# Performance work log

Hardware: AMD Instinct MI355X
Metric: run time of the kernel (lower is better)

The kernel has to match this reference:

```python
import jax, jax.numpy as jnp
import numpy as np

DEPTH, DIM, HEADS, DHEAD, MLP, CTX_DIM = 4, 1024, 16, 64, 4096, 1024
INNER = HEADS * DHEAD
SCALE = DHEAD ** -0.5
B, N, M = 4, 1024, 2048


def setup_inputs() -> dict:
    key = jax.random.key(0)
    ks = jax.random.split(key, 16)
    w = lambda k, shape: jax.random.normal(k, shape, dtype=jnp.float32) * 0.02
    return {
        "x": jax.random.normal(ks[0], (B, N, DIM), dtype=jnp.float32),
        "context": jax.random.normal(ks[1], (B, M, CTX_DIM), dtype=jnp.float32),
        "mask": jnp.ones((B, N), dtype=jnp.int32),
        # LayerNorm params: index 0 = pre-self-attn, 1 = pre-cross-attn, 2 = pre-FFN
        "ln_g": jnp.ones((DEPTH, 3, DIM), dtype=jnp.float32),
        "ln_b": jnp.zeros((DEPTH, 3, DIM), dtype=jnp.float32),
        "Wqkv": w(ks[2], (DEPTH, DIM, 3 * INNER)),
        "Wo_sa": w(ks[3], (DEPTH, INNER, DIM)),
        "bo_sa": jnp.zeros((DEPTH, DIM), dtype=jnp.float32),
        "Wkv": w(ks[4], (DEPTH, CTX_DIM, 2 * INNER)),
        "Wq": w(ks[5], (DEPTH, DIM, INNER)),
        "Wo_ca": w(ks[6], (DEPTH, INNER, DIM)),
        "bo_ca": jnp.zeros((DEPTH, DIM), dtype=jnp.float32),
        "W1": w(ks[7], (DEPTH, DIM, MLP)),
        "b1": jnp.zeros((DEPTH, MLP), dtype=jnp.float32),
        "W2": w(ks[8], (DEPTH, MLP, DIM)),
        "b2": jnp.zeros((DEPTH, DIM), dtype=jnp.float32),
    }


def _ln(x, g, b, eps=1e-5):
    mu = jnp.mean(x, axis=-1, keepdims=True)
    var = jnp.var(x, axis=-1, keepdims=True)
    return (x - mu) * jax.lax.rsqrt(var + eps) * g + b


def _split_heads(t):  # [b, n, h*d] -> [b, h, n, d]
    b, n, _ = t.shape
    return t.reshape(b, n, HEADS, DHEAD).transpose(0, 2, 1, 3)


def _merge_heads(t):  # [b, h, n, d] -> [b, n, h*d]
    b, h, n, d = t.shape
    return t.transpose(0, 2, 1, 3).reshape(b, n, h * d)


def _forward(x, context, mask, ln_g, ln_b, Wqkv, Wo_sa, bo_sa, Wkv, Wq, Wo_ca, bo_ca, W1, b1, W2, b2):
    neg_mask = (1 - mask).astype(x.dtype)  # [b, n]
    for i in range(DEPTH):
        # ---- self-attention (PreNorm) ----
        h = _ln(x, ln_g[i, 0], ln_b[i, 0])
        qkv = h @ Wqkv[i]
        q, k, v = jnp.split(qkv, 3, axis=-1)
        q, k, v = _split_heads(q), _split_heads(k), _split_heads(v)
        dots = jnp.einsum('bhnd,bhmd->bhnm', q, k) * SCALE
        dots = dots - neg_mask[:, None, None, :] * 1e11  # mask over keys
        attn = jax.nn.softmax(dots, axis=-1)
        out = _merge_heads(jnp.einsum('bhnm,bhmd->bhnd', attn, v))
        x = x + out @ Wo_sa[i] + bo_sa[i]
        # ---- cross-attention (PreNorm) ----
        h = _ln(x, ln_g[i, 1], ln_b[i, 1])
        kv = context @ Wkv[i]
        k, v = jnp.split(kv, 2, axis=-1)
        q = _split_heads(h @ Wq[i])
        k, v = _split_heads(k), _split_heads(v)
        dots = jnp.einsum('bhnd,bhmd->bhnm', q, k) * SCALE  # [b, h, n, m]
        dots = dots - neg_mask[:, None, :, None] * 1e6  # mask over queries
        attn = jax.nn.softmax(dots, axis=-1)
        out = _merge_heads(jnp.einsum('bhnm,bhmd->bhnd', attn, v))
        x = x + out @ Wo_ca[i] + bo_ca[i]
        # ---- feed-forward (PreNorm) ----
        h = _ln(x, ln_g[i, 2], ln_b[i, 2])
        h = jax.nn.gelu(h @ W1[i] + b1[i], approximate=False)
        x = x + h @ W2[i] + b2[i]
    return x


def reference(x, context, mask, ln_g, ln_b, Wqkv, Wo_sa, bo_sa, Wkv, Wq, Wo_ca, bo_ca, W1, b1, W2, b2):
    return _forward(x, context, mask, ln_g, ln_b, Wqkv, Wo_sa, bo_sa, Wkv, Wq, Wo_ca, bo_ca, W1, b1, W2, b2)
```

## Files before the change

kernel.cpp:

```cpp
#include <hip/hip_runtime.h>
#include <math.h>

#define DEPTH_ 4
#define DIM_ 1024
#define HEADS_ 16
#define DHEAD_ 64
#define MLP_ 4096
#define CTX_ 1024
#define INNER_ 1024
#define B_ 4
#define N_ 1024
#define M_ 2048

typedef unsigned short u16;
typedef __attribute__((ext_vector_type(4))) unsigned short u16x4;
typedef __attribute__((ext_vector_type(8))) short bf16x8;
typedef __attribute__((ext_vector_type(4))) float f32x4;
typedef __attribute__((ext_vector_type(4))) int i32x4;

#define SCQ 0.18033688011112042f

__device__ __forceinline__ u16 f2bf(float f) {
    unsigned u = __float_as_uint(f);
    return (u16)((u + 0x7fffu + ((u >> 16) & 1u)) >> 16);
}

__device__ __forceinline__ float bf2f(u16 v) {
    return __uint_as_float(((unsigned)v) << 16);
}

__device__ __forceinline__ float exp2_fast(float x) {
    float r;
    asm("v_exp_f32 %0, %1" : "=v"(r) : "v"(x));
    return r;
}

__device__ __forceinline__ float rcp_fast(float x) {
    float r;
    asm("v_rcp_f32 %0, %1" : "=v"(r) : "v"(x));
    return r;
}

__device__ __forceinline__ float max3f(float a, float b, float c) {
    float r;
    asm("v_max3_f32 %0, %1, %2, %3" : "=v"(r) : "v"(a), "v"(b), "v"(c));
    return r;
}

__device__ __forceinline__ unsigned cvt_pk_bf16(float lo, float hi) {
    unsigned r;
    asm("v_cvt_pk_bf16_f32 %0, %1, %2" : "=v"(r) : "v"(lo), "v"(hi));
    return r;
}

__device__ __forceinline__ float gelu_fast(float v) {
    float t = v + 0.044715f * v * v * v;
    float e = exp2_fast(-2.302221673f * t);
    return v * rcp_fast(1.0f + e);
}

__device__ __forceinline__ int kv_sigma(int kv) {
    return (kv & ~31) | (((kv >> 2) & 3) << 3) | (((kv >> 4) & 1) << 2) |
           (kv & 3);
}

#define GLOAD16(gp, sp)                                                        \
    __builtin_amdgcn_global_load_lds(                                          \
        (const __attribute__((address_space(1))) void*)(gp),                   \
        (__attribute__((address_space(3))) void*)(sp), 16, 0, 0)

template <int MODE>
__global__ __launch_bounds__(256) void ln_res(
    u16* __restrict__ xb, const u16* __restrict__ d0,
    const u16* __restrict__ d1, const float* __restrict__ dbias,
    const float* __restrict__ g, const float* __restrict__ b,
    u16* __restrict__ y) {
    int row = blockIdx.x;
    u16x4 xv = ((const u16x4*)(xb + (size_t)row * DIM_))[threadIdx.x];
    float4 v = {bf2f(xv[0]), bf2f(xv[1]), bf2f(xv[2]), bf2f(xv[3])};
    if constexpr (MODE == 1) {
        u16x4 a0 = ((const u16x4*)(d0 + (size_t)row * DIM_))[threadIdx.x];
        u16x4 a1 = ((const u16x4*)(d1 + (size_t)row * DIM_))[threadIdx.x];
        float4 bb4 = ((const float4*)dbias)[threadIdx.x];
        v.x += bf2f(a0[0]) + bf2f(a1[0]) + bb4.x;
        v.y += bf2f(a0[1]) + bf2f(a1[1]) + bb4.y;
        v.z += bf2f(a0[2]) + bf2f(a1[2]) + bb4.z;
        v.w += bf2f(a0[3]) + bf2f(a1[3]) + bb4.w;
        u16x4 xo = {f2bf(v.x), f2bf(v.y), f2bf(v.z), f2bf(v.w)};
        ((u16x4*)(xb + (size_t)row * DIM_))[threadIdx.x] = xo;
    }
    float s  = v.x + v.y + v.z + v.w;
    float ss = v.x * v.x + v.y * v.y + v.z * v.z + v.w * v.w;
    #pragma unroll
    for (int off = 32; off; off >>= 1) {
        s  += __shfl_down(s, off);
        ss += __shfl_down(ss, off);
    }
    __shared__ float red[10];
    int wid = threadIdx.x >> 6, lane = threadIdx.x & 63;
    if (lane == 0) { red[wid] = s; red[4 + wid] = ss; }
    __syncthreads();
    if (threadIdx.x == 0) {
        float ts  = red[0] + red[1] + red[2] + red[3];
        float tss = red[4] + red[5] + red[6] + red[7];
        float mu  = ts * (1.0f / DIM_);
        float var = tss * (1.0f / DIM_) - mu * mu;
        red[8] = mu;
        red[9] = rsqrtf(var + 1e-5f);
    }
    __syncthreads();
    float mu = red[8], rs = red[9];
    float4 gg = ((const float4*)g)[threadIdx.x];
    float4 bb = ((const float4*)b)[threadIdx.x];
    u16x4 o;
    o[0] = f2bf((v.x - mu) * rs * gg.x + bb.x);
    o[1] = f2bf((v.y - mu) * rs * gg.y + bb.y);
    o[2] = f2bf((v.z - mu) * rs * gg.z + bb.z);
    o[3] = f2bf((v.w - mu) * rs * gg.w + bb.w);
    ((u16x4*)(y + (size_t)row * DIM_))[threadIdx.x] = o;
}

__global__ __launch_bounds__(256) void res_add(
    float* __restrict__ xout, const u16* __restrict__ xb,
    const u16* __restrict__ d0, const u16* __restrict__ d1,
    const float* __restrict__ dbias) {
    int row = blockIdx.x;
    u16x4 xv = ((const u16x4*)(xb + (size_t)row * DIM_))[threadIdx.x];
    u16x4 a0 = ((const u16x4*)(d0 + (size_t)row * DIM_))[threadIdx.x];
    u16x4 a1 = ((const u16x4*)(d1 + (size_t)row * DIM_))[threadIdx.x];
    float4 bb4 = ((const float4*)dbias)[threadIdx.x];
    float4 v;
    v.x = bf2f(xv[0]) + bf2f(a0[0]) + bf2f(a1[0]) + bb4.x;
    v.y = bf2f(xv[1]) + bf2f(a0[1]) + bf2f(a1[1]) + bb4.y;
    v.z = bf2f(xv[2]) + bf2f(a0[2]) + bf2f(a1[2]) + bb4.z;
    v.w = bf2f(xv[3]) + bf2f(a0[3]) + bf2f(a1[3]) + bb4.w;
    ((float4*)(xout + (size_t)row * DIM_))[threadIdx.x] = v;
}

__global__ __launch_bounds__(256) void cast_kernel(const float* __restrict__ in,
                                                   u16* __restrict__ out) {
    int i = blockIdx.x * 256 + threadIdx.x;
    float4 v = ((const float4*)in)[i];
    u16x4 o = {f2bf(v.x), f2bf(v.y), f2bf(v.z), f2bf(v.w)};
    ((u16x4*)out)[i] = o;
}

struct PrepArgs {
    const float* src[7];
    int K[7];
    int N[7];
    int dstOff[7];
    int tileCum[7];
};

__global__ __launch_bounds__(256) void prep_weights(PrepArgs a,
                                                    u16* __restrict__ wt) {
    __shared__ float tile[32][33];
    int bid = blockIdx.x;
    int wi = 0;
    while (bid >= a.tileCum[wi]) ++wi;
    int tbase = wi ? a.tileCum[wi - 1] : 0;
    int tid = bid - tbase;
    int Kd = a.K[wi], Nd = a.N[wi];
    int ntx = Nd >> 5;
    int bx = (tid % ntx) * 32;
    int by = (tid / ntx) * 32;
    const float* W = a.src[wi];
    u16* Wt = wt + a.dstOff[wi];

    int t = threadIdx.x;
    int kl = t >> 3, n4 = (t & 7) * 4;
    float4 v = *(const float4*)(W + (size_t)(by + kl) * Nd + bx + n4);
    tile[kl][n4 + 0] = v.x; tile[kl][n4 + 1] = v.y;
    tile[kl][n4 + 2] = v.z; tile[kl][n4 + 3] = v.w;
    __syncthreads();
    int nl = t >> 3, k4 = (t & 7) * 4;
    u16x4 o;
    #pragma unroll
    for (int j = 0; j < 4; ++j) o[j] = f2bf(tile[k4 + j][nl]);
    *(u16x4*)(Wt + (size_t)(bx + nl) * Kd + by + k4) = o;
}

template <int EPI, int SPLITK>
__global__ __launch_bounds__(256, 3) void gemm_mfma3(
    const u16* __restrict__ A, const u16* __restrict__ Bt,
    const float* __restrict__ bias, void* __restrict__ Cout,
    u16* __restrict__ vt, int Mdim, int Ndim, int Kdim, int nx, int ny) {
    __shared__ __align__(16) u16 As[3][128 * 32];
    __shared__ __align__(16) u16 Bs[3][128 * 32];
    const int t = threadIdx.x;
    const int lane = t & 63, w = t >> 6;
    const int c = lane & 15, g = lane >> 4;
    const int wy = w >> 1, wx = w & 1;

    const int nwg = gridDim.x;
    const int wid = (blockIdx.x & 7) * (nwg >> 3) + (blockIdx.x >> 3);
    const int bx = wid % nx;
    const int by = (wid / nx) % ny;
    const int bz = wid / (nx * ny);
    const int m0 = by * 128, n0 = bx * 128;

    f32x4 acc[4][4] = {};

    const int srow = w * 32 + (lane >> 2);
    const int scb  = (((lane & 3) ^ ((srow >> 1) & 3)) * 8);
    const u16* Ag = A + (size_t)(m0 + srow) * Kdim + scb;
    const u16* Bg = Bt + (size_t)(n0 + srow) * Kdim + scb;

    auto stage = [&](int buf, int k0) {
        GLOAD16(Ag + k0, &As[buf][w * 1024]);
        GLOAD16(Ag + k0 + (size_t)16 * Kdim, &As[buf][w * 1024 + 512]);
        GLOAD16(Bg + k0, &Bs[buf][w * 1024]);
        GLOAD16(Bg + k0 + (size_t)16 * Kdim, &Bs[buf][w * 1024 + 512]);
    };
    const int rsw = (c >> 1) & 3;
    auto compute = [&](int buf) {
        bf16x8 a[4], b[4];
        #pragma unroll
        for (int i = 0; i < 4; ++i)
            a[i] = *(const bf16x8*)&As[buf][(wy * 64 + i * 16 + c) * 32 +
                                            ((g ^ rsw) * 8)];
        #pragma unroll
        for (int j = 0; j < 4; ++j)
            b[j] = *(const bf16x8*)&Bs[buf][(wx * 64 + j * 16 + c) * 32 +
                                            ((g ^ rsw) * 8)];
        __builtin_amdgcn_s_setprio(1);
        #pragma unroll
        for (int i = 0; i < 4; ++i)
            #pragma unroll
            for (int j = 0; j < 4; ++j)
                acc[i][j] = __builtin_amdgcn_mfma_f32_16x16x32_bf16(
                    a[i], b[j], acc[i][j], 0, 0, 0);
        __builtin_amdgcn_s_setprio(0);
    };

    const int kchunk = Kdim / SPLITK;
    const int kbeg = bz * kchunk;
    const int nsteps = kchunk / 32;

    stage(0, kbeg);
    stage(1, kbeg + 32);
    int cb = 0, sb = 2;
    for (int s = 0; s < nsteps; ++s) {
        if (s + 1 < nsteps)
            asm volatile("s_waitcnt vmcnt(4)" ::: "memory");
        else
            asm volatile("s_waitcnt vmcnt(0)" ::: "memory");
        __builtin_amdgcn_s_barrier();
        if (s + 2 < nsteps) {
            stage(sb, kbeg + (s + 2) * 32);
            sb = (sb == 2) ? 0 : sb + 1;
        }
        compute(cb);
        cb = (cb == 2) ? 0 : cb + 1;
    }

    const size_t outOff = (SPLITK > 1) ? (size_t)bz * Mdim * Ndim : 0;

    #pragma unroll
    for (int i = 0; i < 4; ++i) {
        int row0 = m0 + wy * 64 + i * 16 + g * 4;
        #pragma unroll
        for (int j = 0; j < 4; ++j) {
            int col = n0 + wx * 64 + j * 16 + c;
            u16x4 o4;
            #pragma unroll
            for (int r = 0; r < 4; ++r) {
                float v = acc[i][j][r];
                size_t idx = (size_t)(row0 + r) * Ndim + col;
                if constexpr (EPI == 0) {
                    ((u16*)Cout)[outOff + idx] = f2bf(v);
                } else if constexpr (EPI == 4) {
                    if (col < 1024) {
                        ((u16*)Cout)[idx] = f2bf(v * SCQ);
                    } else if (col < 2048) {
                        ((u16*)Cout)[idx] = f2bf(v);
                    } else {
                        o4[r] = f2bf(v);
                    }
                } else if constexpr (EPI == 1) {
                    v += bias[col];
                    ((u16*)Cout)[idx] = f2bf(gelu_fast(v));
                }
            }
            if constexpr (EPI == 4) {
                if (n0 + wx * 64 + j * 16 >= 2048) {
                    int hh = (col - 2048) >> 6;
                    int dd = col & 63;
                    int bi = row0 / 1024;
                    int kv = row0 % 1024;
                    int kvs = kv_sigma(kv);
                    *(u16x4*)&vt[(((size_t)bi * HEADS_ + hh) * 64 + dd) * 1024 +
                                 kvs] = o4;
                }
            }
        }
    }
}

__global__ __launch_bounds__(256, 3) void gemm_dual(
    const u16* __restrict__ Akv, const u16* __restrict__ Btkv,
    u16* __restrict__ Ckv, u16* __restrict__ vt,
    const u16* __restrict__ Aq, const u16* __restrict__ Btq,
    u16* __restrict__ Cq) {
    __shared__ __align__(16) u16 As[3][128 * 32];
    __shared__ __align__(16) u16 Bs[3][128 * 32];
    const int t = threadIdx.x;
    const int lane = t & 63, w = t >> 6;
    const int c = lane & 15, g = lane >> 4;
    const int wy = w >> 1, wx = w & 1;
    const int Kdim = 1024;

    const int nwg = gridDim.x;
    const int wid = (blockIdx.x & 7) * (nwg >> 3) + (blockIdx.x >> 3);
    const bool pkv = wid < 1024;
    const u16* A;
    const u16* Bt;
    u16* Cc;
    int Ndim, bx, by;
    if (pkv) {
        A = Akv; Bt = Btkv; Cc = Ckv; Ndim = 2048;
        bx = wid & 15; by = wid >> 4;
    } else {
        int w2 = wid - 1024;
        A = Aq; Bt = Btq; Cc = Cq; Ndim = 1024;
        bx = w2 & 7; by = w2 >> 3;
    }
    const int m0 = by * 128, n0 = bx * 128;

    f32x4 acc[4][4] = {};

    const int srow = w * 32 + (lane >> 2);
    const int scb  = (((lane & 3) ^ ((srow >> 1) & 3)) * 8);
    const u16* Ag = A + (size_t)(m0 + srow) * Kdim + scb;
    const u16* Bg = Bt + (size_t)(n0 + srow) * Kdim + scb;

    auto stage = [&](int buf, int k0) {
        GLOAD16(Ag + k0, &As[buf][w * 1024]);
        GLOAD16(Ag + k0 + (size_t)16 * Kdim, &As[buf][w * 1024 + 512]);
        GLOAD16(Bg + k0, &Bs[buf][w * 1024]);
        GLOAD16(Bg + k0 + (size_t)16 * Kdim, &Bs[buf][w * 1024 + 512]);
    };
    const int rsw = (c >> 1) & 3;
    auto compute = [&](int buf) {
        bf16x8 a[4], b[4];
        #pragma unroll
        for (int i = 0; i < 4; ++i)
            a[i] = *(const bf16x8*)&As[buf][(wy * 64 + i * 16 + c) * 32 +
                                            ((g ^ rsw) * 8)];
        #pragma unroll
        for (int j = 0; j < 4; ++j)
            b[j] = *(const bf16x8*)&Bs[buf][(wx * 64 + j * 16 + c) * 32 +
                                            ((g ^ rsw) * 8)];
        __builtin_amdgcn_s_setprio(1);
        #pragma unroll
        for (int i = 0; i < 4; ++i)
            #pragma unroll
            for (int j = 0; j < 4; ++j)
                acc[i][j] = __builtin_amdgcn_mfma_f32_16x16x32_bf16(
                    a[i], b[j], acc[i][j], 0, 0, 0);
        __builtin_amdgcn_s_setprio(0);
    };

    stage(0, 0);
    stage(1, 32);
    int cb = 0, sb = 2;
    const int nsteps = 32;
    for (int s = 0; s < nsteps; ++s) {
        if (s + 1 < nsteps)
            asm volatile("s_waitcnt vmcnt(4)" ::: "memory");
        else
            asm volatile("s_waitcnt vmcnt(0)" ::: "memory");
        __builtin_amdgcn_s_barrier();
        if (s + 2 < nsteps) {
            stage(sb, (s + 2) * 32);
            sb = (sb == 2) ? 0 : sb + 1;
        }
        compute(cb);
        cb = (cb == 2) ? 0 : cb + 1;
    }

    #pragma unroll
    for (int i = 0; i < 4; ++i) {
        int row0 = m0 + wy * 64 + i * 16 + g * 4;
        #pragma unroll
        for (int j = 0; j < 4; ++j) {
            int col = n0 + wx * 64 + j * 16 + c;
            u16x4 o4;
            #pragma unroll
            for (int r = 0; r < 4; ++r) {
                float v = acc[i][j][r];
                size_t idx = (size_t)(row0 + r) * Ndim + col;
                if (pkv) {
                    u16 bv = f2bf(v);
                    if (col < 1024) Cc[idx] = bv;
                    o4[r] = bv;
                } else {
                    Cc[idx] = f2bf(v * SCQ);
                }
            }
            if (pkv && (n0 + wx * 64 + j * 16 >= 1024)) {
                int hh = (col - 1024) >> 6;
                int dd = col & 63;
                int bi = row0 / 2048;
                int kv = row0 % 2048;
                int kvs = kv_sigma(kv);
                *(u16x4*)&vt[(((size_t)bi * HEADS_ + hh) * 64 + dd) * 2048 +
                             kvs] = o4;
            }
        }
    }
}

template <int KLEN, int IS_SA>
__global__ __launch_bounds__(256) void attn_mfma2(
    const u16* __restrict__ Qsrc, const u16* __restrict__ Ksrc,
    const u16* __restrict__ Vtg, const int* __restrict__ mask,
    u16* __restrict__ O) {
    constexpr int QSTR = IS_SA ? 3 * INNER_ : INNER_;
    constexpr int KSTR = IS_SA ? 3 * INNER_ : 2 * INNER_;
    constexpr int KOFF = IS_SA ? INNER_ : 0;

    __shared__ __align__(16) u16 Ks[3][64 * 64];
    __shared__ __align__(16) u16 Vs[3][64 * 64];

    const int t = threadIdx.x;
    const int lane = t & 63, w = t >> 6;
    const int c = lane & 15, g = lane >> 4;

    const int nwg = gridDim.x;
    const int wid = (blockIdx.x & 7) * (nwg >> 3) + (blockIdx.x >> 3);
    const int qb = wid & 15;
    const int h  = (wid >> 4) & 15;
    const int bb = wid >> 8;
    const int q0 = qb * 64;
    const int kvbase = bb * KLEN;

    const u16* qp =
        Qsrc + (size_t)(bb * N_ + q0 + w * 16 + c) * QSTR + h * 64 + g * 8;
    bf16x8 qf[2];
    qf[0] = *(const bf16x8*)qp;
    qf[1] = *(const bf16x8*)(qp + 32);

    const int sl_r = lane >> 3;
    const int scol = ((lane & 7) ^ sl_r) * 8;
    const int r0 = w * 16, r1 = w * 16 + 8;
    const u16* kp0 = Ksrc + (size_t)(kvbase + r0 + sl_r) * KSTR + KOFF +
                     h * 64 + scol;
    const u16* kp1 = Ksrc + (size_t)(kvbase + r1 + sl_r) * KSTR + KOFF +
                     h * 64 + scol;
    const u16* vp0 =
        Vtg + ((size_t)(bb * HEADS_ + h) * 64 + r0 + sl_r) * KLEN + scol;
    const u16* vp1 =
        Vtg + ((size_t)(bb * HEADS_ + h) * 64 + r1 + sl_r) * KLEN + scol;
    const int* mp = mask + bb * N_ + lane;

    auto stageKV = [&](int buf) {
        GLOAD16(kp0, &Ks[buf][r0 * 64]);
        GLOAD16(kp1, &Ks[buf][r1 * 64]);
        GLOAD16(vp0, &Vs[buf][r0 * 64]);
        GLOAD16(vp1, &Vs[buf][r1 * 64]);
        kp0 += (size_t)64 * KSTR;
        kp1 += (size_t)64 * KSTR;
        vp0 += 64;
        vp1 += 64;
    };

    f32x4 o[4] = {};
    f32x4 oL = {};
    float mr = -1e30f;
    const i32x4 onesI = {0x3F803F80, 0x3F803F80, 0x3F803F80, 0x3F803F80};
    const bf16x8 ones = *(const bf16x8*)&onesI;
    constexpr int NT = KLEN / 64;

    stageKV(0);
    stageKV(1);
    int cb = 0, sb = 2;

    for (int kt = 0; kt < NT; ++kt) {
        if (kt + 1 < NT)
            asm volatile("s_waitcnt vmcnt(4)" ::: "memory");
        else
            asm volatile("s_waitcnt vmcnt(0)" ::: "memory");
        __builtin_amdgcn_s_barrier();
        if (kt + 2 < NT) {
            stageKV(sb);
            sb = (sb == 2) ? 0 : sb + 1;
        }

        f32x4 sv[4] = {};
        #pragma unroll
        for (int kvb = 0; kvb < 4; ++kvb) {
            #pragma unroll
            for (int f = 0; f < 2; ++f) {
                bf16x8 kf = *(const bf16x8*)&Ks[cb][(kvb * 16 + c) * 64 +
                                                    (((g + 4 * f) ^ (c & 7)) * 8)];
                sv[kvb] = __builtin_amdgcn_mfma_f32_16x16x32_bf16(
                    kf, qf[f], sv[kvb], 0, 0, 0);
            }
        }

        if constexpr (IS_SA) {
            int mbit = *mp;
            mp += 64;
            unsigned long long ball = __ballot(mbit != 0);
            if (ball != ~0ull) {
                float negm_reg = mbit ? 0.f : 2.0e10f;
                #pragma unroll
                for (int kvb = 0; kvb < 4; ++kvb)
                    #pragma unroll
                    for (int r = 0; r < 4; ++r)
                        sv[kvb][r] -= __shfl(negm_reg, kvb * 16 + g * 4 + r);
            }
        }

        float x0 = max3f(sv[0][0], sv[0][1], sv[0][2]);
        float x1 = max3f(sv[0][3], sv[1][0], sv[1][1]);
        float x2 = max3f(sv[1][2], sv[1][3], sv[2][0]);
        float x3 = max3f(sv[2][1], sv[2][2], sv[2][3]);
        float x4 = max3f(sv[3][0], sv[3][1], sv[3][2]);
        float tm = fmaxf(max3f(x0, x1, x2), max3f(x3, x4, sv[3][3]));

        if (!__all(tm - mr <= 8.0f)) {
            float tmc = fmaxf(tm, __shfl_xor(tm, 16));
            tmc = fmaxf(tmc, __shfl_xor(tmc, 32));
            float mn = fmaxf(mr, tmc);
            float corr = exp2_fast(mr - mn);
            mr = mn;
            float corrO[4];
            #pragma unroll
            for (int r = 0; r < 4; ++r) corrO[r] = __shfl(corr, g * 4 + r);
            #pragma unroll
            for (int db = 0; db < 4; ++db)
                #pragma unroll
                for (int r = 0; r < 4; ++r) o[db][r] *= corrO[r];
            #pragma unroll
            for (int r = 0; r < 4; ++r) oL[r] *= corrO[r];
        }

        #pragma unroll
        for (int kvb = 0; kvb < 4; ++kvb)
            #pragma unroll
            for (int r = 0; r < 4; ++r)
                sv[kvb][r] = exp2_fast(sv[kvb][r] - mr);

        unsigned pk[4][2];
        #pragma unroll
        for (int kvb = 0; kvb < 4; ++kvb)
            #pragma unroll
            for (int j = 0; j < 2; ++j)
                pk[kvb][j] = cvt_pk_bf16(sv[kvb][2 * j], sv[kvb][2 * j + 1]);

        #pragma unroll
        for (int pv = 0; pv < 2; ++pv) {
            i32x4 tw = {(int)pk[2 * pv][0], (int)pk[2 * pv][1],
                        (int)pk[2 * pv + 1][0], (int)pk[2 * pv + 1][1]};
            bf16x8 pa = *(bf16x8*)&tw;
            oL = __builtin_amdgcn_mfma_f32_16x16x32_bf16(pa, ones, oL, 0, 0, 0);
            #pragma unroll
            for (int db = 0; db < 4; ++db) {
                bf16x8 vf = *(const bf16x8*)&Vs[cb][(db * 16 + c) * 64 +
                                                    (((g + 4 * pv) ^ (c & 7)) * 8)];
                o[db] = __builtin_amdgcn_mfma_f32_16x16x32_bf16(pa, vf, o[db],
                                                                0, 0, 0);
            }
        }
        cb = (cb == 2) ? 0 : cb + 1;
    }

    float invO[4];
    #pragma unroll
    for (int r = 0; r < 4; ++r) invO[r] = rcp_fast(oL[r]);
    #pragma unroll
    for (int db = 0; db < 4; ++db)
        #pragma unroll
        for (int r = 0; r < 4; ++r) {
            size_t idx =
                (size_t)(bb * N_ + q0 + w * 16 + g * 4 + r) * INNER_ +
                h * 64 + db * 16 + c;
            O[idx] = f2bf(o[db][r] * invO[r]);
        }
}

extern "C" void kernel_launch(void* const* d_in, const int* in_sizes, int n_in,
                              void* d_out, int out_size, void* d_ws,
                              size_t ws_size, hipStream_t stream) {
    const float* x     = (const float*)d_in[0];
    const float* ctx   = (const float*)d_in[1];
    const int*   mask  = (const int*)d_in[2];
    const float* ln_g  = (const float*)d_in[3];
    const float* ln_b  = (const float*)d_in[4];
    const float* Wqkv  = (const float*)d_in[5];
    const float* Wo_sa = (const float*)d_in[6];
    const float* bo_sa = (const float*)d_in[7];
    const float* Wkv   = (const float*)d_in[8];
    const float* Wq    = (const float*)d_in[9];
    const float* Wo_ca = (const float*)d_in[10];
    const float* bo_ca = (const float*)d_in[11];
    const float* W1    = (const float*)d_in[12];
    const float* b1    = (const float*)d_in[13];
    const float* W2    = (const float*)d_in[14];
    const float* b2    = (const float*)d_in[15];
    float* xout = (float*)d_out;

    char* ws = (char*)d_ws;
    u16* lnout = (u16*)ws;
    u16* big   = (u16*)(ws + (8ull << 20));
    u16* qca   = (u16*)(ws + (40ull << 20));
    u16* ctxb  = (u16*)(ws + (48ull << 20));
    u16* wt    = (u16*)(ws + (64ull << 20));
    u16* xb    = (u16*)(ws + (96ull << 20));
    u16* R1    = (u16*)(ws + (104ull << 20));
    u16* aout  = lnout;

    const int O_QKV = 0;
    const int O_WOSA = 3145728;
    const int O_WQ   = 4194304;
    const int O_WKV  = 5242880;
    const int O_WOCA = 7340032;
    const int O_W1   = 8388608;
    const int O_W2   = 12582912;

    cast_kernel<<<B_ * M_ * CTX_ / 1024, 256, 0, stream>>>(ctx, ctxb);
    cast_kernel<<<B_ * N_ * DIM_ / 1024, 256, 0, stream>>>(x, xb);

    const int ROWS = B_ * N_;
    const int HALF = ROWS * DIM_;
    dim3 blk(256);

    for (int i = 0; i < DEPTH_; ++i) {
        const float* g  = ln_g + (size_t)(i * 3) * DIM_;
        const float* bb = ln_b + (size_t)(i * 3) * DIM_;

        PrepArgs pa;
        pa.src[0] = Wqkv  + (size_t)i * DIM_ * 3 * INNER_;
        pa.src[1] = Wo_sa + (size_t)i * INNER_ * DIM_;
        pa.src[2] = Wq    + (size_t)i * DIM_ * INNER_;
        pa.src[3] = Wkv   + (size_t)i * CTX_ * 2 * INNER_;
        pa.src[4] = Wo_ca + (size_t)i * INNER_ * DIM_;
        pa.src[5] = W1    + (size_t)i * DIM_ * MLP_;
        pa.src[6] = W2    + (size_t)i * MLP_ * DIM_;
        int Ks_[7] = {1024, 1024, 1024, 1024, 1024, 1024, 4096};
        int Ns_[7] = {3072, 1024, 1024, 2048, 1024, 4096, 1024};
        int Of_[7] = {O_QKV, O_WOSA, O_WQ, O_WKV, O_WOCA, O_W1, O_W2};
        int cum = 0;
        for (int k = 0; k < 7; ++k) {
            pa.K[k] = Ks_[k]; pa.N[k] = Ns_[k]; pa.dstOff[k] = Of_[k];
            cum += (Ks_[k] / 32) * (Ns_[k] / 32);
            pa.tileCum[k] = cum;
        }
        prep_weights<<<cum, blk, 0, stream>>>(pa, wt);

        if (i == 0)
            ln_res<0><<<ROWS, blk, 0, stream>>>(xb, nullptr, nullptr,
                                                nullptr, g, bb, lnout);
        else
            ln_res<1><<<ROWS, blk, 0, stream>>>(xb, R1, R1 + HALF,
                                                b2 + (size_t)(i - 1) * DIM_,
                                                g, bb, lnout);
        gemm_mfma3<4, 1><<<24 * 32, blk, 0, stream>>>(
            lnout, wt + O_QKV, nullptr, big, R1, ROWS, 3 * INNER_, DIM_,
            24, 32);
        attn_mfma2<N_, 1><<<1024, blk, 0, stream>>>(big, big, R1, mask,
                                                    aout);
        gemm_mfma3<0, 2><<<8 * 32 * 2, blk, 0, stream>>>(
            aout, wt + O_WOSA, nullptr, R1, nullptr, ROWS, DIM_, INNER_,
            8, 32);

        ln_res<1><<<ROWS, blk, 0, stream>>>(xb, R1, R1 + HALF,
                                            bo_sa + (size_t)i * DIM_,
                                            g + DIM_, bb + DIM_, lnout);
        gemm_dual<<<1280, blk, 0, stream>>>(ctxb, wt + O_WKV, big, R1,
                                            lnout, wt + O_WQ, qca);
        attn_mfma2<M_, 0><<<1024, blk, 0, stream>>>(qca, big, R1, mask,
                                                    aout);
        gemm_mfma3<0, 2><<<8 * 32 * 2, blk, 0, stream>>>(
            aout, wt + O_WOCA, nullptr, R1, nullptr, ROWS, DIM_, INNER_,
            8, 32);

        ln_res<1><<<ROWS, blk, 0, stream>>>(xb, R1, R1 + HALF,
                                            bo_ca + (size_t)i * DIM_,
                                            g + 2 * DIM_, bb + 2 * DIM_,
                                            lnout);
        gemm_mfma3<1, 1><<<32 * 32, blk, 0, stream>>>(
            lnout, wt + O_W1, b1 + (size_t)i * MLP_, big, nullptr, ROWS, MLP_,
            DIM_, 32, 32);
        gemm_mfma3<0, 2><<<8 * 32 * 2, blk, 0, stream>>>(
            big, wt + O_W2, nullptr, R1, nullptr, ROWS, DIM_, MLP_, 8, 32);
    }
    res_add<<<ROWS, blk, 0, stream>>>(xout, xb, R1, R1 + HALF,
                                      b2 + (size_t)(DEPTH_ - 1) * DIM_);
}
```

Baseline: 1.546 ms.

## Process two query tiles per attention workgroup to reuse staged K/V

The attention kernel now handles 128 queries per workgroup instead of 64. Each wave keeps two independent sets of Q fragments, softmax state and output accumulators, and reuses every K/V fragment it reads from LDS for both. This halves global K/V staging traffic and LDS reads per unit of work, and gives more independent MFMA chains to hide latency. The cost is roughly double the accumulator registers, which may lower occupancy, and half as many workgroups (512), which may underfill the GPU.

```diff
diff --git a/kernel.cpp b/kernel.cpp
--- a/kernel.cpp
+++ b/kernel.cpp
@@ -413,7 +413,7 @@
 }
 
 template <int KLEN, int IS_SA>
-__global__ __launch_bounds__(256) void attn_mfma2(
+__global__ __launch_bounds__(256) void attn_mfma3(
     const u16* __restrict__ Qsrc, const u16* __restrict__ Ksrc,
     const u16* __restrict__ Vtg, const int* __restrict__ mask,
     u16* __restrict__ O) {
@@ -430,17 +430,20 @@
 
     const int nwg = gridDim.x;
     const int wid = (blockIdx.x & 7) * (nwg >> 3) + (blockIdx.x >> 3);
-    const int qb = wid & 15;
-    const int h  = (wid >> 4) & 15;
-    const int bb = wid >> 8;
-    const int q0 = qb * 64;
+    const int qb = wid & 7;
+    const int h  = (wid >> 3) & 15;
+    const int bb = wid >> 7;
+    const int q0 = qb * 128;
     const int kvbase = bb * KLEN;
 
-    const u16* qp =
+    const u16* qp0 =
         Qsrc + (size_t)(bb * N_ + q0 + w * 16 + c) * QSTR + h * 64 + g * 8;
-    bf16x8 qf[2];
-    qf[0] = *(const bf16x8*)qp;
-    qf[1] = *(const bf16x8*)(qp + 32);
+    const u16* qp1 = qp0 + (size_t)64 * QSTR;
+    bf16x8 qf0[2], qf1[2];
+    qf0[0] = *(const bf16x8*)qp0;
+    qf0[1] = *(const bf16x8*)(qp0 + 32);
+    qf1[0] = *(const bf16x8*)qp1;
+    qf1[1] = *(const bf16x8*)(qp1 + 32);
 
     const int sl_r = lane >> 3;
     const int scol = ((lane & 7) ^ sl_r) * 8;
@@ -466,9 +469,9 @@
         vp1 += 64;
     };
 
-    f32x4 o[4] = {};
-    f32x4 oL = {};
-    float mr = -1e30f;
+    f32x4 o0[4] = {}, o1[4] = {};
+    f32x4 oL0 = {}, oL1 = {};
+    float mr0 = -1e30f, mr1 = -1e30f;
     const i32x4 onesI = {0x3F803F80, 0x3F803F80, 0x3F803F80, 0x3F803F80};
     const bf16x8 ones = *(const bf16x8*)&onesI;
     constexpr int NT = KLEN / 64;
@@ -483,94 +486,132 @@
         else
             asm volatile("s_waitcnt vmcnt(0)" ::: "memory");
         __builtin_amdgcn_s_barrier();
+        int mbit = 1;
+        if constexpr (IS_SA) {
+            mbit = *mp;
+            mp += 64;
+        }
         if (kt + 2 < NT) {
             stageKV(sb);
             sb = (sb == 2) ? 0 : sb + 1;
         }
 
-        f32x4 sv[4] = {};
+        f32x4 sv0[4] = {}, sv1[4] = {};
         #pragma unroll
         for (int kvb = 0; kvb < 4; ++kvb) {
             #pragma unroll
             for (int f = 0; f < 2; ++f) {
                 bf16x8 kf = *(const bf16x8*)&Ks[cb][(kvb * 16 + c) * 64 +
                                                     (((g + 4 * f) ^ (c & 7)) * 8)];
-                sv[kvb] = __builtin_amdgcn_mfma_f32_16x16x32_bf16(
-                    kf, qf[f], sv[kvb], 0, 0, 0);
+                sv0[kvb] = __builtin_amdgcn_mfma_f32_16x16x32_bf16(
+                    kf, qf0[f], sv0[kvb], 0, 0, 0);
+                sv1[kvb] = __builtin_amdgcn_mfma_f32_16x16x32_bf16(
+                    kf, qf1[f], sv1[kvb], 0, 0, 0);
             }
         }
 
         if constexpr (IS_SA) {
-            int mbit = *mp;
-            mp += 64;
             unsigned long long ball = __ballot(mbit != 0);
             if (ball != ~0ull) {
                 float negm_reg = mbit ? 0.f : 2.0e10f;
                 #pragma unroll
                 for (int kvb = 0; kvb < 4; ++kvb)
                     #pragma unroll
-                    for (int r = 0; r < 4; ++r)
-                        sv[kvb][r] -= __shfl(negm_reg, kvb * 16 + g * 4 + r);
-            }
-        }
-
-        float x0 = max3f(sv[0][0], sv[0][1], sv[0][2]);
-        float x1 = max3f(sv[0][3], sv[1][0], sv[1][1]);
-        float x2 = max3f(sv[1][2], sv[1][3], sv[2][0]);
-        float x3 = max3f(sv[2][1], sv[2][2], sv[2][3]);
-        float x4 = max3f(sv[3][0], sv[3][1], sv[3][2]);
-        float tm = fmaxf(max3f(x0, x1, x2), max3f(x3, x4, sv[3][3]));
-
-        if (!__all(tm - mr <= 8.0f)) {
-            float tmc = fmaxf(tm, __shfl_xor(tm, 16));
-            tmc = fmaxf(tmc, __shfl_xor(tmc, 32));
-            float mn = fmaxf(mr, tmc);
-            float corr = exp2_fast(mr - mn);
-            mr = mn;
-            float corrO[4];
-            #pragma unroll
-            for (int r = 0; r < 4; ++r) corrO[r] = __shfl(corr, g * 4 + r);
+                    for (int r = 0; r < 4; ++r) {
+                        float nm = __shfl(negm_reg, kvb * 16 + g * 4 + r);
+                        sv0[kvb][r] -= nm;
+                        sv1[kvb][r] -= nm;
+                    }
+            }
+        }
+
+        float a0 = max3f(sv0[0][0], sv0[0][1], sv0[0][2]);
+        float a1 = max3f(sv0[0][3], sv0[1][0], sv0[1][1]);
+        float a2 = max3f(sv0[1][2], sv0[1][3], sv0[2][0]);
+        float a3 = max3f(sv0[2][1], sv0[2][2], sv0[2][3]);
+        float a4 = max3f(sv0[3][0], sv0[3][1], sv0[3][2]);
+        float tm0 = fmaxf(max3f(a0, a1, a2), max3f(a3, a4, sv0[3][3]));
+        float b0 = max3f(sv1[0][0], sv1[0][1], sv1[0][2]);
+        float b1 = max3f(sv1[0][3], sv1[1][0], sv1[1][1]);
+        float b2 = max3f(sv1[1][2], sv1[1][3], sv1[2][0]);
+        float b3 = max3f(sv1[2][1], sv1[2][2], sv1[2][3]);
+        float b4 = max3f(sv1[3][0], sv1[3][1], sv1[3][2]);
+        float tm1 = fmaxf(max3f(b0, b1, b2), max3f(b3, b4, sv1[3][3]));
+
+        if (!__all(fmaxf(tm0 - mr0, tm1 - mr1) <= 8.0f)) {
+            float t0 = fmaxf(tm0, __shfl_xor(tm0, 16));
+            t0 = fmaxf(t0, __shfl_xor(t0, 32));
+            float t1 = fmaxf(tm1, __shfl_xor(tm1, 16));
+            t1 = fmaxf(t1, __shfl_xor(t1, 32));
+            float mn0 = fmaxf(mr0, t0), mn1 = fmaxf(mr1, t1);
+            float c0 = exp2_fast(mr0 - mn0), c1 = exp2_fast(mr1 - mn1);
+            mr0 = mn0; mr1 = mn1;
+            float c0O[4], c1O[4];
+            #pragma unroll
+            for (int r = 0; r < 4; ++r) {
+                c0O[r] = __shfl(c0, g * 4 + r);
+                c1O[r] = __shfl(c1, g * 4 + r);
+            }
             #pragma unroll
             for (int db = 0; db < 4; ++db)
                 #pragma unroll
-                for (int r = 0; r < 4; ++r) o[db][r] *= corrO[r];
-            #pragma unroll
-            for (int r = 0; r < 4; ++r) oL[r] *= corrO[r];
+                for (int r = 0; r < 4; ++r) {
+                    o0[db][r] *= c0O[r];
+                    o1[db][r] *= c1O[r];
+                }
+            #pragma unroll
+            for (int r = 0; r < 4; ++r) {
+                oL0[r] *= c0O[r];
+                oL1[r] *= c1O[r];
+            }
         }
 
         #pragma unroll
         for (int kvb = 0; kvb < 4; ++kvb)
             #pragma unroll
-            for (int r = 0; r < 4; ++r)
-                sv[kvb][r] = exp2_fast(sv[kvb][r] - mr);
-
-        unsigned pk[4][2];
+            for (int r = 0; r < 4; ++r) {
+                sv0[kvb][r] = exp2_fast(sv0[kvb][r] - mr0);
+                sv1[kvb][r] = exp2_fast(sv1[kvb][r] - mr1);
+            }
+
+        unsigned pk0[4][2], pk1[4][2];
         #pragma unroll
         for (int kvb = 0; kvb < 4; ++kvb)
             #pragma unroll
-            for (int j = 0; j < 2; ++j)
-                pk[kvb][j] = cvt_pk_bf16(sv[kvb][2 * j], sv[kvb][2 * j + 1]);
+            for (int j = 0; j < 2; ++j) {
+                pk0[kvb][j] = cvt_pk_bf16(sv0[kvb][2 * j], sv0[kvb][2 * j + 1]);
+                pk1[kvb][j] = cvt_pk_bf16(sv1[kvb][2 * j], sv1[kvb][2 * j + 1]);
+            }
 
         #pragma unroll
         for (int pv = 0; pv < 2; ++pv) {
-            i32x4 tw = {(int)pk[2 * pv][0], (int)pk[2 * pv][1],
-                        (int)pk[2 * pv + 1][0], (int)pk[2 * pv + 1][1]};
-            bf16x8 pa = *(bf16x8*)&tw;
-            oL = __builtin_amdgcn_mfma_f32_16x16x32_bf16(pa, ones, oL, 0, 0, 0);
+            i32x4 tw0 = {(int)pk0[2 * pv][0], (int)pk0[2 * pv][1],
+                         (int)pk0[2 * pv + 1][0], (int)pk0[2 * pv + 1][1]};
+            i32x4 tw1 = {(int)pk1[2 * pv][0], (int)pk1[2 * pv][1],
+                         (int)pk1[2 * pv + 1][0], (int)pk1[2 * pv + 1][1]};
+            bf16x8 pa0 = *(bf16x8*)&tw0;
+            bf16x8 pa1 = *(bf16x8*)&tw1;
+            oL0 = __builtin_amdgcn_mfma_f32_16x16x32_bf16(pa0, ones, oL0, 0, 0, 0);
+            oL1 = __builtin_amdgcn_mfma_f32_16x16x32_bf16(pa1, ones, oL1, 0, 0, 0);
             #pragma unroll
             for (int db = 0; db < 4; ++db) {
                 bf16x8 vf = *(const bf16x8*)&Vs[cb][(db * 16 + c) * 64 +
                                                     (((g + 4 * pv) ^ (c & 7)) * 8)];
-                o[db] = __builtin_amdgcn_mfma_f32_16x16x32_bf16(pa, vf, o[db],
-                                                                0, 0, 0);
+                o0[db] = __builtin_amdgcn_mfma_f32_16x16x32_bf16(pa0, vf,
+                                                                 o0[db], 0, 0, 0);
+                o1[db] = __builtin_amdgcn_mfma_f32_16x16x32_bf16(pa1, vf,
+                                                                 o1[db], 0, 0, 0);
             }
         }
         cb = (cb == 2) ? 0 : cb + 1;
     }
 
-    float invO[4];
+    float i0[4], i1[4];
     #pragma unroll
-    for (int r = 0; r < 4; ++r) invO[r] = rcp_fast(oL[r]);
+    for (int r = 0; r < 4; ++r) {
+        i0[r] = rcp_fast(oL0[r]);
+        i1[r] = rcp_fast(oL1[r]);
+    }
     #pragma unroll
     for (int db = 0; db < 4; ++db)
         #pragma unroll
@@ -578,7 +619,8 @@
             size_t idx =
                 (size_t)(bb * N_ + q0 + w * 16 + g * 4 + r) * INNER_ +
                 h * 64 + db * 16 + c;
-            O[idx] = f2bf(o[db][r] * invO[r]);
+            O[idx] = f2bf(o0[db][r] * i0[r]);
+            O[idx + (size_t)64 * INNER_] = f2bf(o1[db][r] * i1[r]);
         }
 }
 
@@ -661,8 +703,7 @@
         gemm_mfma3<4, 1><<<24 * 32, blk, 0, stream>>>(
             lnout, wt + O_QKV, nullptr, big, R1, ROWS, 3 * INNER_, DIM_,
             24, 32);
-        attn_mfma2<N_, 1><<<1024, blk, 0, stream>>>(big, big, R1, mask,
-                                                    aout);
+        attn_mfma3<N_, 1><<<512, blk, 0, stream>>>(big, big, R1, mask, aout);
         gemm_mfma3<0, 2><<<8 * 32 * 2, blk, 0, stream>>>(
             aout, wt + O_WOSA, nullptr, R1, nullptr, ROWS, DIM_, INNER_,
             8, 32);
@@ -672,8 +713,7 @@
                                             g + DIM_, bb + DIM_, lnout);
         gemm_dual<<<1280, blk, 0, stream>>>(ctxb, wt + O_WKV, big, R1,
                                             lnout, wt + O_WQ, qca);
-        attn_mfma2<M_, 0><<<1024, blk, 0, stream>>>(qca, big, R1, mask,
-                                                    aout);
+        attn_mfma3<M_, 0><<<512, blk, 0, stream>>>(qca, big, R1, mask, aout);
         gemm_mfma3<0, 2><<<8 * 32 * 2, blk, 0, stream>>>(
             aout, wt + O_WOCA, nullptr, R1, nullptr, ROWS, DIM_, INNER_,
             8, 32);
```

Result: faster. 1.457 ms (-5.7%).
